# Optimization experiments

Measured on AMD Instinct MI355X. Metric: run time of the kernel, lower is better.

Reference implementation:

```python
import jax, jax.numpy as jnp
import numpy as np

NUM_CLASSES = 3
W_CE, W_DICE, W_LOVASZ, W_BOUNDARY, W_TOPO = 0.4, 0.3, 0.2, 0.08, 0.02
DICE_SMOOTH = 1e-5
LOVASZ_SUBSAMPLE_THRESH = 100000
LOVASZ_SUBSAMPLE_N = 50000


def _lovasz_hinge_flat(logits, fg):
    # logits, fg: [N]; fg in {0,1}. Sort errors descending, Lovasz gradient, dot.
    signs = 2.0 * fg - 1.0
    errors = 1.0 - logits * signs
    order = jnp.argsort(-errors)          # descending (stable)
    errors_sorted = errors[order]
    gt_sorted = fg[order]
    gts = gt_sorted.sum()
    intersection = gts - jnp.cumsum(gt_sorted)
    union = gts + jnp.cumsum(1.0 - gt_sorted)
    jaccard = 1.0 - intersection / jnp.maximum(union, 1e-12)
    jaccard = jnp.concatenate([jaccard[:1], jaccard[1:] - jaccard[:-1]])
    grad = jnp.where(gts > 0, jaccard, jnp.zeros_like(jaccard))  # gts==0 -> zero grad
    return jnp.dot(jax.nn.relu(errors_sorted), grad)


def structural_loss(predictions, labels):
    B, C, H, W = predictions.shape
    log_probs = jax.nn.log_softmax(predictions, axis=1)      # [B,C,H,W]
    probs = jnp.exp(log_probs)
    # ---- Cross entropy (mean) and per-pixel CE (reused by boundary loss) ----
    ce_pix = -jnp.take_along_axis(log_probs, labels[:, None, :, :], axis=1)[:, 0]  # [B,H,W]
    ce = ce_pix.mean()
    # ---- Dice loss (flattened over whole batch, per class) ----
    one_hot = jax.nn.one_hot(labels, C, dtype=probs.dtype, axis=1)  # [B,C,H,W]
    inter = jnp.sum(probs * one_hot, axis=(0, 2, 3))                 # [C]
    denom = jnp.sum(probs, axis=(0, 2, 3)) + jnp.sum(one_hot, axis=(0, 2, 3))
    dice_scores = (2.0 * inter + DICE_SMOOTH) / (denom + DICE_SMOOTH)
    dice = 1.0 - dice_scores.mean()
    # ---- Lovasz-Softmax ('present' classes, flat over batch, subsampled) ----
    p_flat = probs.transpose(0, 2, 3, 1).reshape(-1, C)  # [N,C]
    l_flat = labels.reshape(-1)                          # [N]
    N = l_flat.shape[0]
    lov_key = jax.random.key(42)
    losses, weights = [], []
    for c in range(C):
        fg_full = (l_flat == c).astype(probs.dtype)
        present = (fg_full.sum() > 0).astype(probs.dtype)
        logits_full = fg_full - p_flat[:, c]
        if N > LOVASZ_SUBSAMPLE_THRESH:
            idx = jax.random.permutation(jax.random.fold_in(lov_key, c), N)[:LOVASZ_SUBSAMPLE_N]
            logits_c, fg_c = logits_full[idx], fg_full[idx]
        else:
            logits_c, fg_c = logits_full, fg_full
        losses.append(_lovasz_hinge_flat(logits_c, fg_c))
        weights.append(present)
    losses = jnp.stack(losses)
    wts = jnp.stack(weights)
    lovasz = jnp.sum(losses * wts) / jnp.maximum(jnp.sum(wts), 1.0)
    # ---- Boundary loss: np.gradient-style boundary mask on classes {1,2} ----
    bnd = jnp.zeros(labels.shape, dtype=bool)
    for c in (1, 2):
        cm = (labels == c).astype(jnp.float32)          # [B,H,W]
        gx = jnp.abs(jnp.gradient(cm, axis=2))
        gy = jnp.abs(jnp.gradient(cm, axis=1))
        bnd = bnd | ((gx + gy) > 0.1)
    bmask = bnd.astype(predictions.dtype)
    boundary = jnp.sum(ce_pix * bmask) / (jnp.sum(bmask) + 1e-8)
    # ---- Topology loss (component count degenerates to presence indicator) ----
    topo = jnp.asarray(0.0, dtype=predictions.dtype)
    for c in (1, 2):
        gt_comp = jnp.any(labels == c, axis=(1, 2)).astype(predictions.dtype)      # [B]
        pred_comp = jnp.any(probs[:, c] > 0.5, axis=(1, 2)).astype(predictions.dtype)
        topo = topo + jnp.sum(jnp.maximum(pred_comp - gt_comp, 0.0) ** 2)
    topo = topo / B
    return (W_CE * ce + W_DICE * dice + W_LOVASZ * lovasz
            + W_BOUNDARY * boundary + W_TOPO * topo)


def setup_inputs() -> dict:
    key = jax.random.key(0)
    k1, k2 = jax.random.split(key)
    predictions = jax.random.normal(k1, (16, 3, 1024, 1024), dtype=jnp.float32)
    labels = jax.random.randint(k2, (16, 1024, 1024), 0, 3)
    return {"predictions": predictions, "labels": labels}


def reference(predictions, labels):
    return structural_loss(predictions, labels)
```

## Files before the change

kernel.cpp:

```cpp
#include <hip/hip_runtime.h>
#include <cstdint>
#include <cstddef>

#define K_BINS 512
#define NBLK   2048
#define TPB    256
#define ROWS_PER_BLK 8
#define HW_    1048576u
#define W_     1024u
#define NPIX   16777216u
#define NHIST  (3*K_BINS)
#define NBLK_S (NBLK/8)

#define PA_OFF   0
#define PU_OFF   32768
#define PL_OFF   49152
#define FH_OFF   65536
#define PART_OFF 81920

#define GLD_LDS(SRC, DST)                                                      \
    __builtin_amdgcn_global_load_lds(                                          \
        (const __attribute__((address_space(1))) void*)(SRC),                  \
        (__attribute__((address_space(3))) void*)(DST), 16, 0, 0)

__device__ __forceinline__ void hist_add(unsigned int* h, int c, float e, int isfg) {
    int bin = (int)(e * (float)K_BINS);
    bin = bin < 0 ? 0 : (bin > K_BINS - 1 ? K_BINS - 1 : bin);
    atomicAdd(&h[c * K_BINS + bin], isfg ? 1u : 65536u);
}

__global__ __launch_bounds__(TPB, 4) void k_main(
    const float* __restrict__ pred, const int* __restrict__ lab,
    double* __restrict__ pa, unsigned long long* __restrict__ pu,
    unsigned long long* __restrict__ pl,
    unsigned int* __restrict__ finalhist, unsigned int* __restrict__ part, int use_dump)
{
    __shared__ float spbuf[2][3][1024];
    __shared__ unsigned int h[NHIST];
    __shared__ float redf[2][TPB / 64];
    __shared__ unsigned int redu[TPB / 64];
    __shared__ unsigned long long redl[TPB / 64];

    const int wv   = threadIdx.x >> 6;
    const int lane = threadIdx.x & 63;
    const bool do_hist = ((blockIdx.x & 7u) == 0u);

    const unsigned gr0   = blockIdx.x * ROWS_PER_BLK;
    const unsigned batch = gr0 >> 10;
    const unsigned i0    = gr0 & 1023u;
    const unsigned col   = threadIdx.x * 4u;
    const int*   labimg  = lab  + (size_t)batch * HW_;
    const float* predimg = pred + (size_t)(batch * 3u) * HW_;
    const unsigned bsh = batch * 4u;

#define STAGE(BB, TR)                                                          \
    {                                                                          \
        const unsigned gi = i0 + (unsigned)(TR);                               \
        _Pragma("unroll")                                                      \
        for (int s_ = 0; s_ < 3; ++s_) {                                       \
            const int k_ = wv * 3 + s_;                                        \
            const int c_ = k_ >> 2, q_ = k_ & 3;                               \
            const float* src_ = predimg + (size_t)c_ * HW_ + (size_t)gi * W_   \
                              + (unsigned)(q_ * 256 + lane * 4);               \
            GLD_LDS(src_, &spbuf[BB][c_][q_ * 256]);                           \
        }                                                                      \
    }

#define LROW(RR) (labimg + (size_t)((RR) < 0 ? 0 : ((RR) > 1023 ? 1023 : (RR))) * W_)

    STAGE(0, 0)
    const int ii0 = (int)i0;
    int4 lprev = *(const int4*)(LROW(ii0 - 1) + col);
    int4 lcur  = *(const int4*)(LROW(ii0)     + col);
    int4 lnext = *(const int4*)(LROW(ii0 + 1) + col);
    const bool has_lf = (col > 0u), has_rt = (col < 1020u);
    int lfA = has_lf ? LROW(ii0)[col - 1u] : 0;
    int rtA = has_rt ? LROW(ii0)[col + 4u] : 0;

    if (do_hist) {
        for (int idx = threadIdx.x; idx < NHIST; idx += TPB) h[idx] = 0u;
    }
    __syncthreads();

    float ce_acc = 0.f, bce_acc = 0.f;
    unsigned bcnt = 0;
    unsigned long long fl = 0ull;

#define PIXEL(A0, A1, A2, L, BND)                                              \
        {                                                                      \
            const float a0 = (A0), a1 = (A1), a2 = (A2); const int l = (L);    \
            const float m  = fmaxf(fmaxf(a0, a1), a2);                         \
            const float e0 = __expf(a0 - m), e1 = __expf(a1 - m), e2 = __expf(a2 - m); \
            const float s  = e0 + e1 + e2;                                     \
            const float lse = m + __logf(s);                                   \
            const float al = (l == 0) ? a0 : ((l == 1) ? a1 : a2);             \
            const float ce = lse - al;                                         \
            const float inv = __builtin_amdgcn_rcpf(s);                        \
            const float p0 = e0 * inv, p1 = e1 * inv, p2 = e2 * inv;           \
            ce_acc += ce;                                                      \
            if (BND) { bce_acc += ce; bcnt++; }                                \
            unsigned mbit = (l == 1 ? 1u : 0u) | (l == 2 ? 2u : 0u) |          \
                            (p1 > 0.5f ? 4u : 0u) | (p2 > 0.5f ? 8u : 0u);     \
            fl |= ((unsigned long long)mbit) << bsh;                           \
            if (do_hist) {                                                     \
                hist_add(h, 0, (l == 0) ? p0 : (1.0f - p0), l == 0);           \
                hist_add(h, 1, (l == 1) ? p1 : (1.0f - p1), l == 1);           \
                hist_add(h, 2, (l == 2) ? p2 : (1.0f - p2), l == 2);           \
            }                                                                  \
        }

    for (int r = 0; r < ROWS_PER_BLK; ++r) {
        int4 nlnext = lnext; int nlf = lfA, nrt = rtA;
        if (r < ROWS_PER_BLK - 1) {
            STAGE((r + 1) & 1, r + 1)
            nlnext = *(const int4*)(LROW(ii0 + r + 2) + col);
            nlf = has_lf ? LROW(ii0 + r + 1)[col - 1u] : 0;
            nrt = has_rt ? LROW(ii0 + r + 1)[col + 4u] : 0;
        }

        {
            const float* b0p = spbuf[r & 1][0];
            const float* b1p = spbuf[r & 1][1];
            const float* b2p = spbuf[r & 1][2];
            const float4 C0 = *(const float4*)(b0p + col);
            const float4 C1 = *(const float4*)(b1p + col);
            const float4 C2 = *(const float4*)(b2p + col);
            const int hd0 = (col == 0u)    ? (lcur.x != lcur.y) : (lfA != lcur.y);
            const int hd1 = (lcur.x != lcur.z);
            const int hd2 = (lcur.y != lcur.w);
            const int hd3 = (col == 1020u) ? (lcur.z != lcur.w) : (lcur.z != rtA);
            const int vd0 = (lprev.x != lnext.x), vd1 = (lprev.y != lnext.y);
            const int vd2 = (lprev.z != lnext.z), vd3 = (lprev.w != lnext.w);
            PIXEL(C0.x, C1.x, C2.x, lcur.x, (hd0 | vd0))
            PIXEL(C0.y, C1.y, C2.y, lcur.y, (hd1 | vd1))
            PIXEL(C0.z, C1.z, C2.z, lcur.z, (hd2 | vd2))
            PIXEL(C0.w, C1.w, C2.w, lcur.w, (hd3 | vd3))
        }

        __syncthreads();

        lprev = lcur; lcur = lnext; lnext = nlnext; lfA = nlf; rtA = nrt;
    }
#undef PIXEL
#undef STAGE
#undef LROW

#pragma unroll
    for (int off = 32; off; off >>= 1) {
        ce_acc  += __shfl_down(ce_acc, off);
        bce_acc += __shfl_down(bce_acc, off);
        bcnt    += __shfl_down(bcnt, off);
        fl      |= __shfl_down(fl, off);
    }
    if ((threadIdx.x & 63) == 0) {
        redf[0][wv] = ce_acc; redf[1][wv] = bce_acc;
        redu[wv] = bcnt;
        redl[wv] = fl;
    }
    __syncthreads();
    if (threadIdx.x == 0) {
        double a0 = 0, a1 = 0; unsigned int u = 0; unsigned long long L = 0ull;
        for (int w2 = 0; w2 < TPB / 64; w2++) {
            a0 += (double)redf[0][w2]; a1 += (double)redf[1][w2];
            u += redu[w2]; L |= redl[w2];
        }
        pa[blockIdx.x * 2 + 0] = a0;
        pa[blockIdx.x * 2 + 1] = a1;
        pu[blockIdx.x] = (unsigned long long)u;
        pl[blockIdx.x] = L;
    }

    if (do_hist) {
        __syncthreads();
        if (use_dump) {
            unsigned int* dst = part + (size_t)(blockIdx.x >> 3) * NHIST;
            for (int idx = threadIdx.x; idx < NHIST; idx += TPB) dst[idx] = h[idx];
        } else {
            for (int idx = threadIdx.x; idx < NHIST; idx += TPB) {
                unsigned int v = h[idx];
                if (v & 0xFFFFu)  atomicAdd(&finalhist[idx * 2 + 0], v & 0xFFFFu);
                if (v >> 16)      atomicAdd(&finalhist[idx * 2 + 1], v >> 16);
            }
        }
    }
}

__global__ __launch_bounds__(256) void k_reduce(const unsigned int* __restrict__ part,
                                               unsigned int* __restrict__ finalhist)
{
    const int f = blockIdx.x * 256 + threadIdx.x;
    unsigned int lo = 0, hi = 0;
    for (int blk = 0; blk < NBLK_S; ++blk) {
        const unsigned int v = part[(size_t)blk * NHIST + f];
        lo += v & 0xFFFFu;
        hi += v >> 16;
    }
    finalhist[f * 2 + 0] = lo;
    finalhist[f * 2 + 1] = hi;
}

__global__ __launch_bounds__(1024) void k_final(
    const double* __restrict__ pa, const unsigned long long* __restrict__ pu,
    const unsigned long long* __restrict__ pl,
    const unsigned int* __restrict__ finalhist, float* __restrict__ out)
{
    __shared__ unsigned int sf[K_BINS], sb[K_BINS];
    __shared__ double red[16];
    __shared__ double red4[16][4];
    __shared__ double lres[3];
    __shared__ double dInter[3], dSumP[3], dCnt[3];
    __shared__ double tot[3];
    __shared__ unsigned long long totL;
    const int t = threadIdx.x;

    {
        double a0 = pa[t * 2 + 0] + pa[(t + 1024) * 2 + 0];
        double a1 = pa[t * 2 + 1] + pa[(t + 1024) * 2 + 1];
        double uu = (double)pu[t] + (double)pu[t + 1024];
        unsigned long long L = pl[t] | pl[t + 1024];
#pragma unroll
        for (int off = 32; off; off >>= 1) {
            a0 += __shfl_down(a0, off);
            a1 += __shfl_down(a1, off);
            uu += __shfl_down(uu, off);
            L  |= __shfl_down(L, off);
        }
        if ((t & 63) == 0) { red4[t >> 6][0] = a0; red4[t >> 6][1] = a1;
                             red4[t >> 6][2] = uu;
                             red[t >> 6] = __longlong_as_double((long long)L); }
        __syncthreads();
        if (t == 0) {
            double s0 = 0, s1 = 0, s2 = 0; unsigned long long LL = 0ull;
            for (int w2 = 0; w2 < 16; ++w2) {
                s0 += red4[w2][0]; s1 += red4[w2][1]; s2 += red4[w2][2];
                LL |= (unsigned long long)__double_as_longlong(red[w2]);
            }
            tot[0] = s0; tot[1] = s1; tot[2] = s2; totL = LL;
        }
        __syncthreads();
    }

    for (int c = 0; c < 3; ++c) {
        unsigned int fgc = 0, bgc = 0;
        if (t < K_BINS) {
            fgc = finalhist[(c * K_BINS + t) * 2 + 0];
            bgc = finalhist[(c * K_BINS + t) * 2 + 1];
            sf[t] = fgc; sb[t] = bgc;
        }
        const double ec = ((double)t + 0.5) / (double)K_BINS;
        double s0 = (t < K_BINS) ? (double)fgc : 0.0;
        double s1 = (t < K_BINS) ? (double)fgc * ec : 0.0;
        double s2 = (t < K_BINS) ? (double)bgc : 0.0;
        double s3 = (t < K_BINS) ? (double)bgc * ec : 0.0;
#pragma unroll
        for (int off = 32; off; off >>= 1) {
            s0 += __shfl_down(s0, off); s1 += __shfl_down(s1, off);
            s2 += __shfl_down(s2, off); s3 += __shfl_down(s3, off);
        }
        if ((t & 63) == 0) { red4[t >> 6][0] = s0; red4[t >> 6][1] = s1;
                             red4[t >> 6][2] = s2; red4[t >> 6][3] = s3; }
        __syncthreads();
        if (t == 0) {
            double cntf = 0, sfe = 0, cntb = 0, sbe = 0;
            for (int w2 = 0; w2 < 16; ++w2) {
                cntf += red4[w2][0]; sfe += red4[w2][1];
                cntb += red4[w2][2]; sbe += red4[w2][3];
            }
            const double inter = sfe;
            dInter[c] = inter;
            dSumP[c]  = inter + (cntb - sbe);
            dCnt[c]   = cntf;
        }
        __syncthreads();

        for (int off = 1; off < K_BINS; off <<= 1) {
            unsigned int vf = 0, vb = 0;
            if (t < K_BINS) {
                vf = sf[t] + ((t + off < K_BINS) ? sf[t + off] : 0u);
                vb = sb[t] + ((t + off < K_BINS) ? sb[t + off] : 0u);
            }
            __syncthreads();
            if (t < K_BINS) { sf[t] = vf; sb[t] = vb; }
            __syncthreads();
        }
        const unsigned int gtsu = sf[0];
        double Jk = 0.0;
        if (t >= 1 && t < K_BINS && gtsu > 0u) {
            const double gts = (double)gtsu;
            Jk = 1.0 - (gts - (double)sf[t]) / (gts + (double)sb[t]);
        }
#pragma unroll
        for (int off = 32; off; off >>= 1) Jk += __shfl_down(Jk, off);
        if ((t & 63) == 0) red[t >> 6] = Jk;
        __syncthreads();
        if (t == 0) {
            double sj = 0; for (int w2 = 0; w2 < 16; ++w2) sj += red[w2];
            lres[c] = (gtsu > 0u) ? ((0.5 + sj) / (double)K_BINS) : -1.0;
        }
        __syncthreads();
    }

    if (t == 0) {
        const double N = 16777216.0;
        const double ce = tot[0] / N;
        double dsum = 0.0;
        for (int c = 0; c < 3; c++) {
            dsum += (2.0 * dInter[c] + 1e-5) / (dSumP[c] + dCnt[c] + 1e-5);
        }
        const double dice = 1.0 - dsum / 3.0;
        double lsum = 0.0, wsum = 0.0;
        for (int c = 0; c < 3; c++) {
            if (lres[c] >= 0.0) { lsum += lres[c]; wsum += 1.0; }
        }
        const double lovasz = lsum / fmax(wsum, 1.0);
        const double bnd = tot[1] / (tot[2] + 1e-8);
        const unsigned long long fl = totL;
        double topo = 0.0;
        for (int b = 0; b < 16; b++) {
            for (int c2 = 0; c2 < 2; c2++) {
                const double gt = (double)((fl >> (b * 4 + c2)) & 1ull);
                const double pr = (double)((fl >> (b * 4 + 2 + c2)) & 1ull);
                const double d = pr - gt;
                if (d > 0.0) topo += d * d;
            }
        }
        topo /= 16.0;
        out[0] = (float)(0.4 * ce + 0.3 * dice + 0.2 * lovasz + 0.08 * bnd + 0.02 * topo);
    }
}

extern "C" void kernel_launch(void* const* d_in, const int* in_sizes, int n_in,
                              void* d_out, int out_size, void* d_ws, size_t ws_size,
                              hipStream_t stream)
{
    const float* pred = (const float*)d_in[0];
    const int*   lab  = (const int*)d_in[1];
    float* out = (float*)d_out;

    char* wsb = (char*)d_ws;
    double* pa = (double*)(wsb + PA_OFF);
    unsigned long long* pu = (unsigned long long*)(wsb + PU_OFF);
    unsigned long long* pl = (unsigned long long*)(wsb + PL_OFF);
    unsigned int* finalhist = (unsigned int*)(wsb + FH_OFF);
    unsigned int* part = (unsigned int*)(wsb + PART_OFF);
    const size_t need = (size_t)PART_OFF + (size_t)NBLK_S * NHIST * 4u;
    const int use_dump = (ws_size >= need) ? 1 : 0;

    if (!use_dump)
        hipMemsetAsync(finalhist, 0, NHIST * 2 * sizeof(unsigned int), stream);

    hipLaunchKernelGGL(k_main, dim3(NBLK), dim3(TPB), 0, stream,
                       pred, lab, pa, pu, pl, finalhist, part, use_dump);
    if (use_dump)
        hipLaunchKernelGGL(k_reduce, dim3(NHIST / 256), dim3(256), 0, stream, part, finalhist);
    hipLaunchKernelGGL(k_final, dim3(1), dim3(1024), 0, stream, pa, pu, pl, finalhist, out);
}
```

Baseline: 87.14 us.

## Deepen async LDS prefetch to four-stage ring with explicit vmcnt waits

Moves the per-row prediction staging from a double buffer to a 4-slot LDS ring that keeps two rows in flight. Replaces the per-iteration __syncthreads with manual s_waitcnt vmcnt counts plus raw barriers. To fit the larger LDS footprint, it halves the Lovasz histogram bins and lowers the launch-bounds occupancy hint from 4 to 3. The intent is to hide more global-load latency, at the cost of coarser histogram quantization, fewer resident blocks, and fragile hand-counted wait values.

Result: no change. 86.15 us (-1.1%).

```diff
diff --git a/kernel.cpp b/kernel.cpp
--- a/kernel.cpp
+++ b/kernel.cpp
@@ -2,7 +2,7 @@
 #include <cstdint>
 #include <cstddef>
 
-#define K_BINS 512
+#define K_BINS 256
 #define NBLK   2048
 #define TPB    256
 #define ROWS_PER_BLK 8
@@ -29,13 +29,13 @@
     atomicAdd(&h[c * K_BINS + bin], isfg ? 1u : 65536u);
 }
 
-__global__ __launch_bounds__(TPB, 4) void k_main(
+__global__ __launch_bounds__(TPB, 3) void k_main(
     const float* __restrict__ pred, const int* __restrict__ lab,
     double* __restrict__ pa, unsigned long long* __restrict__ pu,
     unsigned long long* __restrict__ pl,
     unsigned int* __restrict__ finalhist, unsigned int* __restrict__ part, int use_dump)
 {
-    __shared__ float spbuf[2][3][1024];
+    __shared__ float spbuf[4][3][1024];
     __shared__ unsigned int h[NHIST];
     __shared__ float redf[2][TPB / 64];
     __shared__ unsigned int redu[TPB / 64];
@@ -53,7 +53,7 @@
     const float* predimg = pred + (size_t)(batch * 3u) * HW_;
     const unsigned bsh = batch * 4u;
 
-#define STAGE(BB, TR)                                                          \
+#define STAGE(TR)                                                              \
     {                                                                          \
         const unsigned gi = i0 + (unsigned)(TR);                               \
         _Pragma("unroll")                                                      \
@@ -62,29 +62,36 @@
             const int c_ = k_ >> 2, q_ = k_ & 3;                               \
             const float* src_ = predimg + (size_t)c_ * HW_ + (size_t)gi * W_   \
                               + (unsigned)(q_ * 256 + lane * 4);               \
-            GLD_LDS(src_, &spbuf[BB][c_][q_ * 256]);                           \
+            GLD_LDS(src_, &spbuf[(TR) & 3][c_][q_ * 256]);                     \
         }                                                                      \
     }
 
 #define LROW(RR) (labimg + (size_t)((RR) < 0 ? 0 : ((RR) > 1023 ? 1023 : (RR))) * W_)
 
-    STAGE(0, 0)
+    if (do_hist) {
+        for (int idx = threadIdx.x; idx < NHIST; idx += TPB) h[idx] = 0u;
+    }
+
     const int ii0 = (int)i0;
+    const bool has_lf = (col > 0u), has_rt = (col < 1020u);
+
     int4 lprev = *(const int4*)(LROW(ii0 - 1) + col);
     int4 lcur  = *(const int4*)(LROW(ii0)     + col);
-    int4 lnext = *(const int4*)(LROW(ii0 + 1) + col);
-    const bool has_lf = (col > 0u), has_rt = (col < 1020u);
-    int lfA = has_lf ? LROW(ii0)[col - 1u] : 0;
-    int rtA = has_rt ? LROW(ii0)[col + 4u] : 0;
-
-    if (do_hist) {
-        for (int idx = threadIdx.x; idx < NHIST; idx += TPB) h[idx] = 0u;
-    }
-    __syncthreads();
+    int4 ln0   = *(const int4*)(LROW(ii0 + 1) + col);
+    int lf0 = has_lf ? LROW(ii0)[col - 1u] : 0;
+    int rt0 = has_rt ? LROW(ii0)[col + 4u] : 0;
+    STAGE(0)
+    asm volatile("" ::: "memory");
+    int4 ln1 = *(const int4*)(LROW(ii0 + 2) + col);
+    int lf1 = has_lf ? LROW(ii0 + 1)[col - 1u] : 0;
+    int rt1 = has_rt ? LROW(ii0 + 1)[col + 4u] : 0;
+    STAGE(1)
+    asm volatile("" ::: "memory");
 
     float ce_acc = 0.f, bce_acc = 0.f;
     unsigned bcnt = 0;
     unsigned long long fl = 0ull;
+    int4 ln2; int lf2, rt2;
 
 #define PIXEL(A0, A1, A2, L, BND)                                              \
         {                                                                      \
@@ -109,39 +116,56 @@
             }                                                                  \
         }
 
-    for (int r = 0; r < ROWS_PER_BLK; ++r) {
-        int4 nlnext = lnext; int nlf = lfA, nrt = rtA;
-        if (r < ROWS_PER_BLK - 1) {
-            STAGE((r + 1) & 1, r + 1)
-            nlnext = *(const int4*)(LROW(ii0 + r + 2) + col);
-            nlf = has_lf ? LROW(ii0 + r + 1)[col - 1u] : 0;
-            nrt = has_rt ? LROW(ii0 + r + 1)[col + 4u] : 0;
-        }
-
-        {
-            const float* b0p = spbuf[r & 1][0];
-            const float* b1p = spbuf[r & 1][1];
-            const float* b2p = spbuf[r & 1][2];
-            const float4 C0 = *(const float4*)(b0p + col);
-            const float4 C1 = *(const float4*)(b1p + col);
-            const float4 C2 = *(const float4*)(b2p + col);
-            const int hd0 = (col == 0u)    ? (lcur.x != lcur.y) : (lfA != lcur.y);
-            const int hd1 = (lcur.x != lcur.z);
-            const int hd2 = (lcur.y != lcur.w);
-            const int hd3 = (col == 1020u) ? (lcur.z != lcur.w) : (lcur.z != rtA);
-            const int vd0 = (lprev.x != lnext.x), vd1 = (lprev.y != lnext.y);
-            const int vd2 = (lprev.z != lnext.z), vd3 = (lprev.w != lnext.w);
-            PIXEL(C0.x, C1.x, C2.x, lcur.x, (hd0 | vd0))
-            PIXEL(C0.y, C1.y, C2.y, lcur.y, (hd1 | vd1))
-            PIXEL(C0.z, C1.z, C2.z, lcur.z, (hd2 | vd2))
-            PIXEL(C0.w, C1.w, C2.w, lcur.w, (hd3 | vd3))
-        }
-
-        __syncthreads();
-
-        lprev = lcur; lcur = lnext; lnext = nlnext; lfA = nlf; rtA = nrt;
-    }
+#define COMPUTE(R)                                                             \
+    {                                                                          \
+        const float* b0p = spbuf[(R) & 3][0];                                  \
+        const float* b1p = spbuf[(R) & 3][1];                                  \
+        const float* b2p = spbuf[(R) & 3][2];                                  \
+        const float4 C0 = *(const float4*)(b0p + col);                         \
+        const float4 C1 = *(const float4*)(b1p + col);                         \
+        const float4 C2 = *(const float4*)(b2p + col);                         \
+        const int hd0 = (col == 0u)    ? (lcur.x != lcur.y) : (lf0 != lcur.y); \
+        const int hd1 = (lcur.x != lcur.z);                                    \
+        const int hd2 = (lcur.y != lcur.w);                                    \
+        const int hd3 = (col == 1020u) ? (lcur.z != lcur.w) : (lcur.z != rt0); \
+        const int vd0 = (lprev.x != ln0.x), vd1 = (lprev.y != ln0.y);          \
+        const int vd2 = (lprev.z != ln0.z), vd3 = (lprev.w != ln0.w);          \
+        PIXEL(C0.x, C1.x, C2.x, lcur.x, (hd0 | vd0))                           \
+        PIXEL(C0.y, C1.y, C2.y, lcur.y, (hd1 | vd1))                           \
+        PIXEL(C0.z, C1.z, C2.z, lcur.z, (hd2 | vd2))                           \
+        PIXEL(C0.w, C1.w, C2.w, lcur.w, (hd3 | vd3))                           \
+    }                                                                          \
+    lprev = lcur; lcur = ln0; ln0 = ln1; ln1 = ln2;                            \
+    lf0 = lf1; rt0 = rt1; lf1 = lf2; rt1 = rt2;
+
+    STAGE(2)
+    ln2 = *(const int4*)(LROW(ii0 + 3) + col);
+    lf2 = has_lf ? LROW(ii0 + 2)[col - 1u] : 0;
+    rt2 = has_rt ? LROW(ii0 + 2)[col + 4u] : 0;
+    asm volatile("s_waitcnt vmcnt(12) lgkmcnt(0)" ::: "memory");
+    __builtin_amdgcn_s_barrier();
+    COMPUTE(0)
+
+    for (int r = 1; r <= ROWS_PER_BLK - 3; ++r) {
+        STAGE(r + 2)
+        ln2 = *(const int4*)(LROW(ii0 + r + 3) + col);
+        lf2 = has_lf ? LROW(ii0 + r + 2)[col - 1u] : 0;
+        rt2 = has_rt ? LROW(ii0 + r + 2)[col + 4u] : 0;
+        asm volatile("s_waitcnt vmcnt(12)" ::: "memory");
+        __builtin_amdgcn_s_barrier();
+        COMPUTE(r)
+    }
+
+    asm volatile("s_waitcnt vmcnt(6)" ::: "memory");
+    __builtin_amdgcn_s_barrier();
+    COMPUTE(ROWS_PER_BLK - 2)
+
+    asm volatile("s_waitcnt vmcnt(0)" ::: "memory");
+    __builtin_amdgcn_s_barrier();
+    COMPUTE(ROWS_PER_BLK - 1)
+
 #undef PIXEL
+#undef COMPUTE
 #undef STAGE
 #undef LROW
 
```
